# Performance work log

Measured on AMD Instinct MI355X. Metric: run time of the kernel, lower is better.

The kernel has to match this reference:

```python
import jax, jax.numpy as jnp
import numpy as np

B, N, DIN, DOUT = 4, 4096, 512, 128
NEG_INF = -1.0e9  # matches torch's -1000000000.0 fill


def setup_inputs() -> dict:
    key = jax.random.key(0)
    k1, k2, k3, k4 = jax.random.split(key, 4)
    x = jax.random.normal(k1, (B, N, DIN), dtype=jnp.float32)
    adj = (jax.random.uniform(k2, (N, N)) < 0.004).astype(jnp.float32)
    # xavier_uniform with gain=sqrt(2) for weights
    lim_w = float(np.sqrt(2.0) * np.sqrt(6.0 / (DIN + DOUT)))
    weights = jax.random.uniform(k3, (DIN, DOUT), jnp.float32, -lim_w, lim_w)
    # xavier_uniform (gain=1) for a: shape [2*DOUT, 1]
    lim_a = float(np.sqrt(6.0 / (2 * DOUT + 1)))
    a = jax.random.uniform(k4, (2 * DOUT, 1), jnp.float32, -lim_a, lim_a)
    return {"x": x, "adj": adj, "weights": weights, "a": a}


def reference(x, adj, weights, a):
    d = weights.shape[1]
    a_src = a[:d]   # [D, 1]
    a_dst = a[d:]   # [D, 1]

    def per_graph(xs):  # xs: [N, DIN]
        wh = xs @ weights                      # [N, D]
        e = wh @ a_src + (wh @ a_dst).T        # [N,1] + [1,N] -> [N,N]
        e = jnp.where(e > 0, e, 0.01 * e)      # LeakyReLU(0.01)
        att = jax.nn.softmax(jnp.where(adj > 0, e, NEG_INF), axis=1)
        out = att @ wh                          # [N, D]
        return adj @ out                        # sparse-adj mm (dense here)

    return jax.nn.relu(jax.vmap(per_graph)(x))  # act = ReLU
```

## Files before the change

kernel.cpp:

```cpp
#include <hip/hip_runtime.h>
#include <hip/hip_bf16.h>
#include <cstdint>
#include <cstddef>

#define BATCH 4
#define NNODE 4096
#define DIN   512
#define DOUT  128
#define CAP   64

typedef __attribute__((ext_vector_type(8))) short bf16x8;
typedef __attribute__((ext_vector_type(4))) float f32x4;

static __device__ __forceinline__ unsigned short f2bf_rne(float f) {
    union { float f; uint32_t u; } v; v.f = f;
    uint32_t u = v.u;
    uint32_t r = u + 0x7FFFu + ((u >> 16) & 1u);
    return (unsigned short)(r >> 16);
}
static __device__ __forceinline__ float bf2f(unsigned short h) {
    union { float f; uint32_t u; } v; v.u = ((uint32_t)h) << 16;
    return v.f;
}

__global__ __launch_bounds__(256) void k_build_csr(const float* __restrict__ adj,
                                                   int* __restrict__ nbr_cnt,
                                                   int* __restrict__ nbr_idx) {
    __shared__ int cnt;
    int row = blockIdx.x;
    if (threadIdx.x == 0) cnt = 0;
    __syncthreads();
    const float4* arow = (const float4*)(adj + (size_t)row * NNODE);
#pragma unroll
    for (int k = 0; k < 4; ++k) {
        int idx4 = threadIdx.x + k * 256;
        float4 v = arow[idx4];
        int cbase = idx4 * 4;
        if (v.x > 0.f) { int p = atomicAdd(&cnt, 1); if (p < CAP) nbr_idx[row*CAP+p] = cbase; }
        if (v.y > 0.f) { int p = atomicAdd(&cnt, 1); if (p < CAP) nbr_idx[row*CAP+p] = cbase+1; }
        if (v.z > 0.f) { int p = atomicAdd(&cnt, 1); if (p < CAP) nbr_idx[row*CAP+p] = cbase+2; }
        if (v.w > 0.f) { int p = atomicAdd(&cnt, 1); if (p < CAP) nbr_idx[row*CAP+p] = cbase+3; }
    }
    __syncthreads();
    if (threadIdx.x == 0) nbr_cnt[row] = cnt > CAP ? CAP : cnt;
}

__global__ __launch_bounds__(256) void k_wt(const float* __restrict__ W,
                                            unsigned short* __restrict__ Wt) {
    __shared__ float tile[32][33];
    int kb = (blockIdx.x >> 2) * 32;
    int nb = (blockIdx.x & 3) * 32;
    int t = threadIdx.x;
#pragma unroll
    for (int r = 0; r < 4; ++r) {
        int kl = r*8 + (t >> 5);
        int nl = t & 31;
        tile[kl][nl] = W[(size_t)(kb+kl)*DOUT + nb+nl];
    }
    __syncthreads();
#pragma unroll
    for (int r = 0; r < 4; ++r) {
        int nl = r*8 + (t >> 5);
        int kl = t & 31;
        Wt[(size_t)(nb+nl)*DIN + kb+kl] = f2bf_rne(tile[kl][nl]);
    }
}

__global__ __launch_bounds__(256) void k_wh(const float* __restrict__ x,
                                            const unsigned short* __restrict__ Wt,
                                            float* __restrict__ wh) {
    int w = threadIdx.x >> 6;
    int l = threadIdx.x & 63;
    int row = blockIdx.x * 64 + w * 16 + (l & 15);
    int kq = (l >> 4) * 8;
    f32x4 acc[8] = {};
    const float* xrow = x + (size_t)row * DIN + kq;
    for (int ks = 0; ks < 16; ++ks) {
        float4 a0 = *(const float4*)(xrow + ks*32);
        float4 a1 = *(const float4*)(xrow + ks*32 + 4);
        float af[8] = {a0.x,a0.y,a0.z,a0.w,a1.x,a1.y,a1.z,a1.w};
        bf16x8 ah, al;
#pragma unroll
        for (int i = 0; i < 8; ++i) {
            unsigned short h = f2bf_rne(af[i]);
            ah[i] = (short)h;
            al[i] = (short)f2bf_rne(af[i] - bf2f(h));
        }
#pragma unroll
        for (int ni = 0; ni < 8; ++ni) {
            int col = ni*16 + (l & 15);
            bf16x8 b = *(const bf16x8*)(Wt + (size_t)col*DIN + ks*32 + kq);
            acc[ni] = __builtin_amdgcn_mfma_f32_16x16x32_bf16(ah, b, acc[ni], 0, 0, 0);
            acc[ni] = __builtin_amdgcn_mfma_f32_16x16x32_bf16(al, b, acc[ni], 0, 0, 0);
        }
    }
    int orow = blockIdx.x*64 + w*16 + (l >> 4)*4;
#pragma unroll
    for (int ni = 0; ni < 8; ++ni) {
        int col = ni*16 + (l & 15);
#pragma unroll
        for (int r = 0; r < 4; ++r)
            wh[(size_t)(orow + r)*DOUT + col] = acc[ni][r];
    }
}

__global__ __launch_bounds__(256) void k_sd(const float* __restrict__ wh,
                                            const float* __restrict__ a,
                                            float* __restrict__ s,
                                            float* __restrict__ d) {
    int row = blockIdx.x * 8 + (threadIdx.x >> 5);
    int l = threadIdx.x & 31;
    float4 w4 = *(const float4*)(wh + (size_t)row*DOUT + l*4);
    float4 as = *(const float4*)(a + l*4);
    float4 ad = *(const float4*)(a + DOUT + l*4);
    float sp = w4.x*as.x + w4.y*as.y + w4.z*as.z + w4.w*as.w;
    float dp = w4.x*ad.x + w4.y*ad.y + w4.z*ad.z + w4.w*ad.w;
#pragma unroll
    for (int off = 16; off >= 1; off >>= 1) {
        sp += __shfl_xor(sp, off, 64);
        dp += __shfl_xor(dp, off, 64);
    }
    if (l == 0) { s[row] = sp; d[row] = dp; }
}

__global__ __launch_bounds__(128) void k_colsum(const float* __restrict__ wh,
                                                float* __restrict__ colsum) {
    int b = blockIdx.x >> 5;
    int chunk = blockIdx.x & 31;
    int col = threadIdx.x;
    const float* base = wh + ((size_t)b*NNODE + chunk*128)*DOUT + col;
    float sum = 0.f;
    for (int r = 0; r < 128; ++r) sum += base[(size_t)r*DOUT];
    atomicAdd(&colsum[b*DOUT + col], sum);
}

__global__ __launch_bounds__(256) void k_att(const float* __restrict__ wh,
                                             const float* __restrict__ s,
                                             const float* __restrict__ dv,
                                             const int* __restrict__ nbr_cnt,
                                             const int* __restrict__ nbr_idx,
                                             const float* __restrict__ colsum,
                                             float* __restrict__ out) {
    int gid = blockIdx.x*4 + (threadIdx.x >> 6);
    int l = threadIdx.x & 63;
    int b = gid >> 12;
    int i = gid & (NNODE-1);
    int c = nbr_cnt[i];
    int j = (l < c) ? nbr_idx[i*CAP + l] : 0;
    float e = -3.0e38f;
    float si = s[gid];
    if (l < c) {
        float ev = si + dv[(b << 12) + j];
        e = ev > 0.f ? ev : 0.01f * ev;
    }
    float m = e;
#pragma unroll
    for (int off = 32; off >= 1; off >>= 1) m = fmaxf(m, __shfl_xor(m, off, 64));
    float p = (l < c) ? __expf(e - m) : 0.f;
    float den = p;
#pragma unroll
    for (int off = 32; off >= 1; off >>= 1) den += __shfl_xor(den, off, 64);
    float2 acc = {0.f, 0.f};
    if (c > 0) {
        float inv = 1.f / den;
        for (int jj = 0; jj < c; ++jj) {
            int jv = __shfl(j, jj, 64);
            float pv = __shfl(p, jj, 64) * inv;
            float2 v = *(const float2*)(wh + ((size_t)((b << 12) + jv))*DOUT + l*2);
            acc.x += pv * v.x;
            acc.y += pv * v.y;
        }
    } else {
        const float inv_n = 1.f / (float)NNODE;
        acc.x = colsum[(b << 7) + l*2]     * inv_n;
        acc.y = colsum[(b << 7) + l*2 + 1] * inv_n;
    }
    *(float2*)(out + (size_t)gid*DOUT + l*2) = acc;
}

__global__ __launch_bounds__(256) void k_agg(const float* __restrict__ out,
                                             const int* __restrict__ nbr_cnt,
                                             const int* __restrict__ nbr_idx,
                                             float* __restrict__ y) {
    int gid = blockIdx.x*4 + (threadIdx.x >> 6);
    int l = threadIdx.x & 63;
    int b = gid >> 12;
    int i = gid & (NNODE-1);
    int c = nbr_cnt[i];
    int j = (l < c) ? nbr_idx[i*CAP + l] : 0;
    float2 acc = {0.f, 0.f};
    for (int jj = 0; jj < c; ++jj) {
        int jv = __shfl(j, jj, 64);
        float2 v = *(const float2*)(out + ((size_t)((b << 12) + jv))*DOUT + l*2);
        acc.x += v.x; acc.y += v.y;
    }
    acc.x = fmaxf(acc.x, 0.f);
    acc.y = fmaxf(acc.y, 0.f);
    *(float2*)(y + (size_t)gid*DOUT + l*2) = acc;
}

extern "C" void kernel_launch(void* const* d_in, const int* in_sizes, int n_in,
                              void* d_out, int out_size, void* d_ws, size_t ws_size,
                              hipStream_t stream) {
    const float* x   = (const float*)d_in[0];
    const float* adj = (const float*)d_in[1];
    const float* W   = (const float*)d_in[2];
    const float* a   = (const float*)d_in[3];
    float* y = (float*)d_out;

    char* ws = (char*)d_ws;
    size_t o = 0;
    int*            nbr_cnt = (int*)(ws + o);            o += (size_t)NNODE*4;
    int*            nbr_idx = (int*)(ws + o);            o += (size_t)NNODE*CAP*4;
    unsigned short* Wt      = (unsigned short*)(ws + o); o += (size_t)DOUT*DIN*2;
    float*          wh      = (float*)(ws + o);          o += (size_t)BATCH*NNODE*DOUT*4;
    float*          sv      = (float*)(ws + o);          o += (size_t)BATCH*NNODE*4;
    float*          dvv     = (float*)(ws + o);          o += (size_t)BATCH*NNODE*4;
    float*          colsum  = (float*)(ws + o);          o += (size_t)BATCH*DOUT*4;
    float*          outbuf  = (float*)(ws + o);          o += (size_t)BATCH*NNODE*DOUT*4;

    hipMemsetAsync(colsum, 0, (size_t)BATCH*DOUT*4, stream);

    k_build_csr<<<NNODE, 256, 0, stream>>>(adj, nbr_cnt, nbr_idx);
    k_wt<<<64, 256, 0, stream>>>(W, Wt);
    k_wh<<<(BATCH*NNODE)/64, 256, 0, stream>>>(x, Wt, wh);
    k_sd<<<(BATCH*NNODE)/8, 256, 0, stream>>>(wh, a, sv, dvv);
    k_colsum<<<BATCH*32, 128, 0, stream>>>(wh, colsum);
    k_att<<<(BATCH*NNODE)/4, 256, 0, stream>>>(wh, sv, dvv, nbr_cnt, nbr_idx, colsum, outbuf);
    k_agg<<<(BATCH*NNODE)/4, 256, 0, stream>>>(outbuf, nbr_cnt, nbr_idx, y);
}
```

Measured before the change: 190.8 us.

## Scan-based CSR build, split-K fused projection, and float4 half-wave gathers

The CSR builder now packs each thread's adjacency hits into a bitmask and places indices with a shared-memory prefix scan instead of per-hit shared atomics. The Wh GEMM splits K across wave pairs, reduces the partial sums through LDS and computes the s/d attention projections in the same kernel, which removes the separate k_sd launch and its reread of Wh. The colsum kernel uses four times as many blocks. The attention and aggregation gathers use float4 loads, with the two half-waves handling alternate neighbours and combining at the end. Together these aim to cut launch count, atomic contention and memory passes, at the cost of extra barriers and LDS traffic.

```diff
diff --git a/kernel.cpp b/kernel.cpp
--- a/kernel.cpp
+++ b/kernel.cpp
@@ -26,23 +26,39 @@
 __global__ __launch_bounds__(256) void k_build_csr(const float* __restrict__ adj,
                                                    int* __restrict__ nbr_cnt,
                                                    int* __restrict__ nbr_idx) {
-    __shared__ int cnt;
+    __shared__ int pref[256];
     int row = blockIdx.x;
-    if (threadIdx.x == 0) cnt = 0;
+    int t = threadIdx.x;
+    const float4* p = (const float4*)(adj + (size_t)row * NNODE) + t * 4;
+    unsigned mask = 0;
+#pragma unroll
+    for (int q = 0; q < 4; ++q) {
+        float4 v = p[q];
+        mask |= (v.x > 0.f ? 1u : 0u) << (q*4+0);
+        mask |= (v.y > 0.f ? 1u : 0u) << (q*4+1);
+        mask |= (v.z > 0.f ? 1u : 0u) << (q*4+2);
+        mask |= (v.w > 0.f ? 1u : 0u) << (q*4+3);
+    }
+    int cnt = __popc(mask);
+    pref[t] = cnt;
     __syncthreads();
-    const float4* arow = (const float4*)(adj + (size_t)row * NNODE);
-#pragma unroll
-    for (int k = 0; k < 4; ++k) {
-        int idx4 = threadIdx.x + k * 256;
-        float4 v = arow[idx4];
-        int cbase = idx4 * 4;
-        if (v.x > 0.f) { int p = atomicAdd(&cnt, 1); if (p < CAP) nbr_idx[row*CAP+p] = cbase; }
-        if (v.y > 0.f) { int p = atomicAdd(&cnt, 1); if (p < CAP) nbr_idx[row*CAP+p] = cbase+1; }
-        if (v.z > 0.f) { int p = atomicAdd(&cnt, 1); if (p < CAP) nbr_idx[row*CAP+p] = cbase+2; }
-        if (v.w > 0.f) { int p = atomicAdd(&cnt, 1); if (p < CAP) nbr_idx[row*CAP+p] = cbase+3; }
-    }
-    __syncthreads();
-    if (threadIdx.x == 0) nbr_cnt[row] = cnt > CAP ? CAP : cnt;
+    for (int off = 1; off < 256; off <<= 1) {
+        int v = pref[t];
+        int add = (t >= off) ? pref[t - off] : 0;
+        __syncthreads();
+        pref[t] = v + add;
+        __syncthreads();
+    }
+    int total = pref[255];
+    int base = pref[t] - cnt;
+    int cbase = t * 16;
+    while (mask) {
+        int b = __ffs(mask) - 1;
+        mask &= mask - 1;
+        if (base < CAP) nbr_idx[row * CAP + base] = cbase + b;
+        ++base;
+    }
+    if (t == 0) nbr_cnt[row] = total > CAP ? CAP : total;
 }
 
 __global__ __launch_bounds__(256) void k_wt(const float* __restrict__ W,
@@ -68,69 +84,97 @@
 
 __global__ __launch_bounds__(256) void k_wh(const float* __restrict__ x,
                                             const unsigned short* __restrict__ Wt,
-                                            float* __restrict__ wh) {
+                                            const float* __restrict__ a,
+                                            float* __restrict__ wh,
+                                            float* __restrict__ sv,
+                                            float* __restrict__ dvv) {
+    __shared__ float lacc[2][8][64][4];
     int w = threadIdx.x >> 6;
     int l = threadIdx.x & 63;
-    int row = blockIdx.x * 64 + w * 16 + (l & 15);
+    int g = w >> 1;
+    int h = w & 1;
+    int rowbase = blockIdx.x * 32 + g * 16;
+    int row = rowbase + (l & 15);
     int kq = (l >> 4) * 8;
     f32x4 acc[8] = {};
-    const float* xrow = x + (size_t)row * DIN + kq;
-    for (int ks = 0; ks < 16; ++ks) {
+    const float* xrow = x + (size_t)row * DIN + h*256 + kq;
+    const unsigned short* wbase = Wt + h*256 + kq;
+    for (int ks = 0; ks < 8; ++ks) {
         float4 a0 = *(const float4*)(xrow + ks*32);
         float4 a1 = *(const float4*)(xrow + ks*32 + 4);
         float af[8] = {a0.x,a0.y,a0.z,a0.w,a1.x,a1.y,a1.z,a1.w};
         bf16x8 ah, al;
 #pragma unroll
         for (int i = 0; i < 8; ++i) {
-            unsigned short h = f2bf_rne(af[i]);
-            ah[i] = (short)h;
-            al[i] = (short)f2bf_rne(af[i] - bf2f(h));
-        }
-#pragma unroll
-        for (int ni = 0; ni < 8; ++ni) {
-            int col = ni*16 + (l & 15);
-            bf16x8 b = *(const bf16x8*)(Wt + (size_t)col*DIN + ks*32 + kq);
+            unsigned short hh = f2bf_rne(af[i]);
+            ah[i] = (short)hh;
+            al[i] = (short)f2bf_rne(af[i] - bf2f(hh));
+        }
+#pragma unroll
+        for (int ni = 0; ni < 8; ++ni) {
+            bf16x8 b = *(const bf16x8*)(wbase + (size_t)(ni*16 + (l & 15))*DIN + ks*32);
             acc[ni] = __builtin_amdgcn_mfma_f32_16x16x32_bf16(ah, b, acc[ni], 0, 0, 0);
             acc[ni] = __builtin_amdgcn_mfma_f32_16x16x32_bf16(al, b, acc[ni], 0, 0, 0);
         }
     }
-    int orow = blockIdx.x*64 + w*16 + (l >> 4)*4;
-#pragma unroll
-    for (int ni = 0; ni < 8; ++ni) {
-        int col = ni*16 + (l & 15);
-#pragma unroll
-        for (int r = 0; r < 4; ++r)
-            wh[(size_t)(orow + r)*DOUT + col] = acc[ni][r];
-    }
-}
-
-__global__ __launch_bounds__(256) void k_sd(const float* __restrict__ wh,
-                                            const float* __restrict__ a,
-                                            float* __restrict__ s,
-                                            float* __restrict__ d) {
-    int row = blockIdx.x * 8 + (threadIdx.x >> 5);
-    int l = threadIdx.x & 31;
-    float4 w4 = *(const float4*)(wh + (size_t)row*DOUT + l*4);
-    float4 as = *(const float4*)(a + l*4);
-    float4 ad = *(const float4*)(a + DOUT + l*4);
-    float sp = w4.x*as.x + w4.y*as.y + w4.z*as.z + w4.w*as.w;
-    float dp = w4.x*ad.x + w4.y*ad.y + w4.z*ad.z + w4.w*ad.w;
-#pragma unroll
-    for (int off = 16; off >= 1; off >>= 1) {
-        sp += __shfl_xor(sp, off, 64);
-        dp += __shfl_xor(dp, off, 64);
-    }
-    if (l == 0) { s[row] = sp; d[row] = dp; }
+    if (h == 1) {
+#pragma unroll
+        for (int ni = 0; ni < 8; ++ni)
+            *(f32x4*)&lacc[g][ni][l][0] = acc[ni];
+    }
+    __syncthreads();
+    if (h == 0) {
+#pragma unroll
+        for (int ni = 0; ni < 8; ++ni) {
+            f32x4 o = *(const f32x4*)&lacc[g][ni][l][0];
+            acc[ni] += o;
+        }
+        float sp[4] = {0,0,0,0}, dp[4] = {0,0,0,0};
+#pragma unroll
+        for (int ni = 0; ni < 8; ++ni) {
+            int col = ni*16 + (l & 15);
+            float as = a[col];
+            float ad = a[DOUT + col];
+#pragma unroll
+            for (int r = 0; r < 4; ++r) {
+                sp[r] += acc[ni][r] * as;
+                dp[r] += acc[ni][r] * ad;
+            }
+        }
+#pragma unroll
+        for (int off = 1; off <= 8; off <<= 1) {
+#pragma unroll
+            for (int r = 0; r < 4; ++r) {
+                sp[r] += __shfl_xor(sp[r], off, 64);
+                dp[r] += __shfl_xor(dp[r], off, 64);
+            }
+        }
+        int row4 = rowbase + (l >> 4) * 4;
+        if ((l & 15) == 0) {
+#pragma unroll
+            for (int r = 0; r < 4; ++r) {
+                sv[row4 + r] = sp[r];
+                dvv[row4 + r] = dp[r];
+            }
+        }
+#pragma unroll
+        for (int ni = 0; ni < 8; ++ni) {
+            int col = ni*16 + (l & 15);
+#pragma unroll
+            for (int r = 0; r < 4; ++r)
+                wh[(size_t)(row4 + r)*DOUT + col] = acc[ni][r];
+        }
+    }
 }
 
 __global__ __launch_bounds__(128) void k_colsum(const float* __restrict__ wh,
                                                 float* __restrict__ colsum) {
-    int b = blockIdx.x >> 5;
-    int chunk = blockIdx.x & 31;
+    int b = blockIdx.x >> 7;
+    int chunk = blockIdx.x & 127;
     int col = threadIdx.x;
-    const float* base = wh + ((size_t)b*NNODE + chunk*128)*DOUT + col;
+    const float* base = wh + ((size_t)b*NNODE + chunk*32)*DOUT + col;
     float sum = 0.f;
-    for (int r = 0; r < 128; ++r) sum += base[(size_t)r*DOUT];
+    for (int r = 0; r < 32; ++r) sum += base[(size_t)r*DOUT];
     atomicAdd(&colsum[b*DOUT + col], sum);
 }
 
@@ -160,22 +204,32 @@
     float den = p;
 #pragma unroll
     for (int off = 32; off >= 1; off >>= 1) den += __shfl_xor(den, off, 64);
-    float2 acc = {0.f, 0.f};
+    int half = l >> 5;
+    int lc = l & 31;
+    float4 acc = {0.f, 0.f, 0.f, 0.f};
     if (c > 0) {
         float inv = 1.f / den;
-        for (int jj = 0; jj < c; ++jj) {
-            int jv = __shfl(j, jj, 64);
-            float pv = __shfl(p, jj, 64) * inv;
-            float2 v = *(const float2*)(wh + ((size_t)((b << 12) + jv))*DOUT + l*2);
-            acc.x += pv * v.x;
-            acc.y += pv * v.y;
-        }
+        for (int jj = 0; jj < c; jj += 2) {
+            int src = jj + half;
+            int jv = __shfl(j, src, 64);
+            float pv = __shfl(p, src, 64) * inv;
+            float4 v = *((const float4*)(wh + ((size_t)((b << 12) + jv))*DOUT) + lc);
+            acc.x += pv * v.x; acc.y += pv * v.y;
+            acc.z += pv * v.z; acc.w += pv * v.w;
+        }
+        acc.x += __shfl_xor(acc.x, 32, 64);
+        acc.y += __shfl_xor(acc.y, 32, 64);
+        acc.z += __shfl_xor(acc.z, 32, 64);
+        acc.w += __shfl_xor(acc.w, 32, 64);
     } else {
         const float inv_n = 1.f / (float)NNODE;
-        acc.x = colsum[(b << 7) + l*2]     * inv_n;
-        acc.y = colsum[(b << 7) + l*2 + 1] * inv_n;
-    }
-    *(float2*)(out + (size_t)gid*DOUT + l*2) = acc;
+        acc.x = colsum[(b << 7) + lc*4]     * inv_n;
+        acc.y = colsum[(b << 7) + lc*4 + 1] * inv_n;
+        acc.z = colsum[(b << 7) + lc*4 + 2] * inv_n;
+        acc.w = colsum[(b << 7) + lc*4 + 3] * inv_n;
+    }
+    if (half == 0)
+        *((float4*)(out + (size_t)gid*DOUT) + lc) = acc;
 }
 
 __global__ __launch_bounds__(256) void k_agg(const float* __restrict__ out,
@@ -188,15 +242,25 @@
     int i = gid & (NNODE-1);
     int c = nbr_cnt[i];
     int j = (l < c) ? nbr_idx[i*CAP + l] : 0;
-    float2 acc = {0.f, 0.f};
-    for (int jj = 0; jj < c; ++jj) {
-        int jv = __shfl(j, jj, 64);
-        float2 v = *(const float2*)(out + ((size_t)((b << 12) + jv))*DOUT + l*2);
-        acc.x += v.x; acc.y += v.y;
-    }
-    acc.x = fmaxf(acc.x, 0.f);
-    acc.y = fmaxf(acc.y, 0.f);
-    *(float2*)(y + (size_t)gid*DOUT + l*2) = acc;
+    int half = l >> 5;
+    int lc = l & 31;
+    float4 acc = {0.f, 0.f, 0.f, 0.f};
+    for (int jj = 0; jj < c; jj += 2) {
+        int src = jj + half;
+        if (src < c) {
+            int jv = __shfl(j, src, 64);
+            float4 v = *((const float4*)(out + ((size_t)((b << 12) + jv))*DOUT) + lc);
+            acc.x += v.x; acc.y += v.y; acc.z += v.z; acc.w += v.w;
+        }
+    }
+    acc.x += __shfl_xor(acc.x, 32, 64);
+    acc.y += __shfl_xor(acc.y, 32, 64);
+    acc.z += __shfl_xor(acc.z, 32, 64);
+    acc.w += __shfl_xor(acc.w, 32, 64);
+    acc.x = fmaxf(acc.x, 0.f); acc.y = fmaxf(acc.y, 0.f);
+    acc.z = fmaxf(acc.z, 0.f); acc.w = fmaxf(acc.w, 0.f);
+    if (half == 0)
+        *((float4*)(y + (size_t)gid*DOUT) + lc) = acc;
 }
 
 extern "C" void kernel_launch(void* const* d_in, const int* in_sizes, int n_in,
@@ -223,9 +287,8 @@
 
     k_build_csr<<<NNODE, 256, 0, stream>>>(adj, nbr_cnt, nbr_idx);
     k_wt<<<64, 256, 0, stream>>>(W, Wt);
-    k_wh<<<(BATCH*NNODE)/64, 256, 0, stream>>>(x, Wt, wh);
-    k_sd<<<(BATCH*NNODE)/8, 256, 0, stream>>>(wh, a, sv, dvv);
-    k_colsum<<<BATCH*32, 128, 0, stream>>>(wh, colsum);
+    k_wh<<<(BATCH*NNODE)/32, 256, 0, stream>>>(x, Wt, a, wh, sv, dvv);
+    k_colsum<<<BATCH*128, 128, 0, stream>>>(wh, colsum);
     k_att<<<(BATCH*NNODE)/4, 256, 0, stream>>>(wh, sv, dvv, nbr_cnt, nbr_idx, colsum, outbuf);
     k_agg<<<(BATCH*NNODE)/4, 256, 0, stream>>>(outbuf, nbr_cnt, nbr_idx, y);
 }
```

Result: faster. 182.0 us (-4.6%).
